# Performance work log

Hardware: AMD Instinct MI355X
Metric: run time of the kernel (lower is better)

The kernel has to match this reference:

```python
import jax, jax.numpy as jnp
import numpy as np

QN, QP = -8.0, 7.0  # int4 quantization range used by the cutlass q4 kernel
SCALE_DENOM = 11.269  # ~sqrt(127), from set_activation_scale


def _quant4(t, clip):
    # clip-based dynamic quantization to int4 grid (values kept in float)
    return jnp.clip(jnp.round(t / clip), QN, QP)


def setup_inputs() -> dict:
    key = jax.random.key(0)
    kx, ky = jax.random.split(key)
    x = jax.random.normal(kx, (4, 16, 1024, 256), dtype=jnp.float32)
    y = jax.random.normal(ky, (4, 16, 256, 1024), dtype=jnp.float32)
    # set_activation_scale: alpha = 2 * |t|.mean() / 11.269 (module uses x for both)
    x_clip = 2.0 * jnp.mean(jnp.abs(x)) / SCALE_DENOM
    y_clip = 2.0 * jnp.mean(jnp.abs(x)) / SCALE_DENOM
    return {"x": x, "y": y, "x_clip": x_clip, "y_clip": y_clip}


def reference(x, y, x_clip, y_clip):
    # quantize both operands to int4 grid, integer-grid matmul, dequant by clip scales
    qx = _quant4(x, x_clip)  # [B, H, M, K]
    qy = _quant4(y, y_clip)  # [B, H, K, N]
    out = jnp.einsum("bhmk,bhkn->bhmn", qx, qy)
    return out * x_clip * y_clip
```

## Files before the change

kernel.cpp:

```cpp
#include <hip/hip_runtime.h>

#define NBATCH 64
#define M_DIM  1024
#define K_DIM  256
#define N_DIM  1024

typedef __attribute__((ext_vector_type(4)))  int   i32x4;
typedef __attribute__((ext_vector_type(4)))  float f32x4;

union Pack16 { char c[16]; i32x4 i; };

__device__ __forceinline__ float quant4f(float v, float clip) {
    return fminf(fmaxf(rintf(v / clip), -8.0f), 7.0f);
}

__global__ __launch_bounds__(256) void quant_kernel(
        const float* __restrict__ x, const float* __restrict__ y,
        const float* __restrict__ xclip_p, const float* __restrict__ yclip_p,
        char* __restrict__ qx, char* __restrict__ qyT) {
    __shared__ float tile[64][65];
    const int bid = blockIdx.x;
    const int tid = threadIdx.x;

    if (bid < 4096) {
        const float clip = xclip_p[0];
        const int idx = (bid * 256 + tid) * 16;
        Pack16 o;
#pragma unroll
        for (int c = 0; c < 4; ++c) {
            f32x4 v = *(const f32x4*)(x + idx + c * 4);
#pragma unroll
            for (int j = 0; j < 4; ++j)
                o.c[c * 4 + j] = (char)(int)quant4f(v[j], clip);
        }
        *(i32x4*)(qx + idx) = o.i;
    } else {
        const float clip = yclip_p[0];
        const int b2 = bid - 4096;
        const int n0 = (b2 & 15) * 64;
        const int kb = (b2 >> 4) & 3;
        const int k0 = kb * 64;
        const int b  = b2 >> 6;
        const float* yb = y + (size_t)b * K_DIM * N_DIM;
        const int kl = tid >> 4;
        const int nq = (tid & 15) * 4;
#pragma unroll
        for (int i = 0; i < 4; ++i) {
            f32x4 v = *(const f32x4*)(yb + (size_t)(k0 + kl + i * 16) * N_DIM + n0 + nq);
#pragma unroll
            for (int j = 0; j < 4; ++j)
                tile[kl + i * 16][nq + j] = quant4f(v[j], clip);
        }
        __syncthreads();
        char* ob = qyT + ((size_t)b * 4 + kb) * 1024 * 64;
        const int nl = tid >> 2;
        const int kc = (tid & 3) * 16;
        Pack16 o;
#pragma unroll
        for (int j = 0; j < 16; ++j)
            o.c[j] = (char)(int)tile[kc + j][nl];
        *(i32x4*)(ob + (size_t)(n0 + nl) * 64 + kc) = o.i;
    }
}

#define GLD16(gp, lp) __builtin_amdgcn_global_load_lds(                         \
    (const __attribute__((address_space(1))) void*)(gp),                        \
    (__attribute__((address_space(3))) void*)(lp), 16, 0, 0)

__global__ __launch_bounds__(256, 4) void q4_gemm_kernel(
        const char* __restrict__ qx,
        const char* __restrict__ qyT,
        const float* __restrict__ xclip_p, const float* __restrict__ yclip_p,
        float* __restrict__ out) {
    const int p = blockIdx.x;
    const int l = (p & 7) * 512 + (p >> 3);
    const int b  = l >> 6;
    const int t  = l & 63;
    const int br = t >> 3;
    const int bc = t & 7;

    __shared__ __align__(16) char smem[32768];
    float (*Cst)[132] = (float (*)[132])smem;

    const int tid  = threadIdx.x;
    const int lane = tid & 63;
    const int wid  = tid >> 6;
    const int wr   = wid >> 1;
    const int wc   = wid & 1;

    const char* Abase = qx  + (size_t)b * M_DIM * K_DIM + (size_t)br * 128 * K_DIM;
    const char* Bbase = qyT + (size_t)b * 4 * 65536 + (size_t)bc * 128 * 64;

    const int row0  = tid >> 2;
    const int row1  = (tid + 256) >> 2;
    const int slot  = tid & 3;
    const int ks0   = (slot ^ (row0 & 3)) * 16;
    const int ks1   = (slot ^ (row1 & 3)) * 16;

    i32x4 acc[4][4] = {};

    const int lrow15 = lane & 15;
    const int s      = lane >> 4;

    {
        char* As = smem; char* Bs = smem + 8192;
        GLD16(Abase + (size_t)row0 * K_DIM + ks0, As + tid * 16);
        GLD16(Bbase + (size_t)row0 * 64 + ks0, Bs + tid * 16);
        GLD16(Abase + (size_t)row1 * K_DIM + ks1, As + (tid + 256) * 16);
        GLD16(Bbase + (size_t)row1 * 64 + ks1, Bs + (tid + 256) * 16);
    }
    __syncthreads();

#pragma unroll
    for (int kt = 0; kt < 4; ++kt) {
        char* As = smem + (kt & 1) * 16384;
        char* Bs = As + 8192;
        if (kt < 3) {
            const int ka = (kt + 1) * 64;
            const size_t kbb = (size_t)(kt + 1) * 65536;
            char* An = smem + ((kt + 1) & 1) * 16384;
            char* Bn = An + 8192;
            GLD16(Abase + (size_t)row0 * K_DIM + ka + ks0, An + tid * 16);
            GLD16(Bbase + kbb + (size_t)row0 * 64 + ks0, Bn + tid * 16);
            GLD16(Abase + (size_t)row1 * K_DIM + ka + ks1, An + (tid + 256) * 16);
            GLD16(Bbase + kbb + (size_t)row1 * 64 + ks1, Bn + (tid + 256) * 16);
        }

        i32x4 af[4], bf[4];
#pragma unroll
        for (int m = 0; m < 4; ++m) {
            int row = wr * 64 + m * 16 + lrow15;
            af[m] = *(const i32x4*)(As + row * 64 + ((s ^ (row & 3)) * 16));
        }
#pragma unroll
        for (int n = 0; n < 4; ++n) {
            int row = wc * 64 + n * 16 + lrow15;
            bf[n] = *(const i32x4*)(Bs + row * 64 + ((s ^ (row & 3)) * 16));
        }
#pragma unroll
        for (int m = 0; m < 4; ++m)
#pragma unroll
            for (int n = 0; n < 4; ++n)
                acc[m][n] = __builtin_amdgcn_mfma_i32_16x16x64_i8(
                                af[m], bf[n], acc[m][n], 0, 0, 0);
        __syncthreads();
    }

    const float scale = xclip_p[0] * yclip_p[0];
    const size_t cb = (size_t)b * M_DIM * N_DIM
                    + (size_t)(br * 128) * N_DIM + bc * 128;
    const int rsub = (lane >> 4) * 4;
    const int rdr  = tid >> 3;
    const int cdw0 = (tid & 7) * 4;

#pragma unroll
    for (int m = 0; m < 4; ++m) {
#pragma unroll
        for (int n = 0; n < 4; ++n)
#pragma unroll
            for (int j = 0; j < 4; ++j)
                Cst[wr * 16 + rsub + j][wc * 64 + n * 16 + lrow15] =
                    (float)acc[m][n][j] * scale;
        __syncthreads();
        const int grow = (rdr >> 4) * 64 + m * 16 + (rdr & 15);
#pragma unroll
        for (int i = 0; i < 4; ++i) {
            f32x4 v = *(const f32x4*)&Cst[rdr][cdw0 + i * 32];
            __builtin_nontemporal_store(
                v, (f32x4*)(out + cb + (size_t)grow * N_DIM + cdw0 + i * 32));
        }
        __syncthreads();
    }
}

extern "C" void kernel_launch(void* const* d_in, const int* in_sizes, int n_in,
                              void* d_out, int out_size, void* d_ws, size_t ws_size,
                              hipStream_t stream) {
    const float* x     = (const float*)d_in[0];
    const float* y     = (const float*)d_in[1];
    const float* xclip = (const float*)d_in[2];
    const float* yclip = (const float*)d_in[3];
    float* out = (float*)d_out;

    char* qx  = (char*)d_ws;
    char* qyT = qx + (size_t)NBATCH * M_DIM * K_DIM;

    quant_kernel<<<8192, 256, 0, stream>>>(x, y, xclip, yclip, qx, qyT);
    q4_gemm_kernel<<<4096, 256, 0, stream>>>(qx, qyT, xclip, yclip, out);
}
```

Before: 79.76 us.

## Fuse x quantization into GEMM tile loading, drop separate qx pass

The separate quantization of x is removed. The GEMM kernel now loads fp32 x tiles directly, quantizes them in registers, and stores packed int8 into swizzled LDS after the MFMA step, overlapping with compute. This avoids writing and rereading the int8 qx buffer. In exchange, each x tile is read in fp32 by every column block (4x the bytes per reuse), register pressure rises, and occupancy hint is lowered to 3.

Measured after the change: 99.69 us. +25.0%, slower.

```diff
diff --git a/kernel.cpp b/kernel.cpp
--- a/kernel.cpp
+++ b/kernel.cpp
@@ -14,61 +14,54 @@
     return fminf(fmaxf(rintf(v / clip), -8.0f), 7.0f);
 }
 
-__global__ __launch_bounds__(256) void quant_kernel(
-        const float* __restrict__ x, const float* __restrict__ y,
-        const float* __restrict__ xclip_p, const float* __restrict__ yclip_p,
-        char* __restrict__ qx, char* __restrict__ qyT) {
+__device__ __forceinline__ i32x4 quant_pack16(const f32x4* v, float clip) {
+    Pack16 o;
+#pragma unroll
+    for (int c = 0; c < 4; ++c)
+#pragma unroll
+        for (int j = 0; j < 4; ++j)
+            o.c[c * 4 + j] = (char)(int)quant4f(v[c][j], clip);
+    return o.i;
+}
+
+__global__ __launch_bounds__(256) void quant_y_kernel(
+        const float* __restrict__ y, const float* __restrict__ clip_p,
+        char* __restrict__ qyT) {
     __shared__ float tile[64][65];
     const int bid = blockIdx.x;
     const int tid = threadIdx.x;
-
-    if (bid < 4096) {
-        const float clip = xclip_p[0];
-        const int idx = (bid * 256 + tid) * 16;
-        Pack16 o;
-#pragma unroll
-        for (int c = 0; c < 4; ++c) {
-            f32x4 v = *(const f32x4*)(x + idx + c * 4);
-#pragma unroll
-            for (int j = 0; j < 4; ++j)
-                o.c[c * 4 + j] = (char)(int)quant4f(v[j], clip);
-        }
-        *(i32x4*)(qx + idx) = o.i;
-    } else {
-        const float clip = yclip_p[0];
-        const int b2 = bid - 4096;
-        const int n0 = (b2 & 15) * 64;
-        const int kb = (b2 >> 4) & 3;
-        const int k0 = kb * 64;
-        const int b  = b2 >> 6;
-        const float* yb = y + (size_t)b * K_DIM * N_DIM;
-        const int kl = tid >> 4;
-        const int nq = (tid & 15) * 4;
-#pragma unroll
-        for (int i = 0; i < 4; ++i) {
-            f32x4 v = *(const f32x4*)(yb + (size_t)(k0 + kl + i * 16) * N_DIM + n0 + nq);
-#pragma unroll
-            for (int j = 0; j < 4; ++j)
-                tile[kl + i * 16][nq + j] = quant4f(v[j], clip);
-        }
-        __syncthreads();
-        char* ob = qyT + ((size_t)b * 4 + kb) * 1024 * 64;
-        const int nl = tid >> 2;
-        const int kc = (tid & 3) * 16;
-        Pack16 o;
-#pragma unroll
-        for (int j = 0; j < 16; ++j)
-            o.c[j] = (char)(int)tile[kc + j][nl];
-        *(i32x4*)(ob + (size_t)(n0 + nl) * 64 + kc) = o.i;
-    }
+    const float clip = clip_p[0];
+    const int n0 = (bid & 15) * 64;
+    const int kb = (bid >> 4) & 3;
+    const int k0 = kb * 64;
+    const int b  = bid >> 6;
+    const float* yb = y + (size_t)b * K_DIM * N_DIM;
+    const int kl = tid >> 4;
+    const int nq = (tid & 15) * 4;
+#pragma unroll
+    for (int i = 0; i < 4; ++i) {
+        f32x4 v = *(const f32x4*)(yb + (size_t)(k0 + kl + i * 16) * N_DIM + n0 + nq);
+#pragma unroll
+        for (int j = 0; j < 4; ++j)
+            tile[kl + i * 16][nq + j] = quant4f(v[j], clip);
+    }
+    __syncthreads();
+    char* ob = qyT + ((size_t)b * 4 + kb) * 1024 * 64;
+    const int nl = tid >> 2;
+    const int kc = (tid & 3) * 16;
+    Pack16 o;
+#pragma unroll
+    for (int j = 0; j < 16; ++j)
+        o.c[j] = (char)(int)tile[kc + j][nl];
+    *(i32x4*)(ob + (size_t)(n0 + nl) * 64 + kc) = o.i;
 }
 
 #define GLD16(gp, lp) __builtin_amdgcn_global_load_lds(                         \
     (const __attribute__((address_space(1))) void*)(gp),                        \
     (__attribute__((address_space(3))) void*)(lp), 16, 0, 0)
 
-__global__ __launch_bounds__(256, 4) void q4_gemm_kernel(
-        const char* __restrict__ qx,
+__global__ __launch_bounds__(256, 3) void q4_gemm_kernel(
+        const float* __restrict__ x,
         const char* __restrict__ qyT,
         const float* __restrict__ xclip_p, const float* __restrict__ yclip_p,
         float* __restrict__ out) {
@@ -88,14 +81,18 @@
     const int wr   = wid >> 1;
     const int wc   = wid & 1;
 
-    const char* Abase = qx  + (size_t)b * M_DIM * K_DIM + (size_t)br * 128 * K_DIM;
-    const char* Bbase = qyT + (size_t)b * 4 * 65536 + (size_t)bc * 128 * 64;
-
-    const int row0  = tid >> 2;
-    const int row1  = (tid + 256) >> 2;
-    const int slot  = tid & 3;
-    const int ks0   = (slot ^ (row0 & 3)) * 16;
-    const int ks1   = (slot ^ (row1 & 3)) * 16;
+    const float* Axf  = x + (size_t)b * M_DIM * K_DIM + (size_t)br * 128 * K_DIM;
+    const char*  Bbase = qyT + (size_t)b * 4 * 65536 + (size_t)bc * 128 * 64;
+    const float  xclip = xclip_p[0];
+
+    const int row0 = tid >> 2;
+    const int row1 = row0 + 64;
+    const int slot = tid & 3;
+    const int ke   = slot * 16;
+    const int wd0  = (slot ^ (row0 & 3)) * 16;
+    const int wd1  = (slot ^ (row1 & 3)) * 16;
+    const int bs0  = wd0;
+    const int bs1  = wd1;
 
     i32x4 acc[4][4] = {};
 
@@ -104,10 +101,16 @@
 
     {
         char* As = smem; char* Bs = smem + 8192;
-        GLD16(Abase + (size_t)row0 * K_DIM + ks0, As + tid * 16);
-        GLD16(Bbase + (size_t)row0 * 64 + ks0, Bs + tid * 16);
-        GLD16(Abase + (size_t)row1 * K_DIM + ks1, As + (tid + 256) * 16);
-        GLD16(Bbase + (size_t)row1 * 64 + ks1, Bs + (tid + 256) * 16);
+        GLD16(Bbase + (size_t)row0 * 64 + bs0, Bs + tid * 16);
+        GLD16(Bbase + (size_t)row1 * 64 + bs1, Bs + (tid + 256) * 16);
+        f32x4 a0[4], a1[4];
+#pragma unroll
+        for (int j = 0; j < 4; ++j) {
+            a0[j] = *(const f32x4*)(Axf + (size_t)row0 * K_DIM + ke + j * 4);
+            a1[j] = *(const f32x4*)(Axf + (size_t)row1 * K_DIM + ke + j * 4);
+        }
+        *(i32x4*)(As + row0 * 64 + wd0) = quant_pack16(a0, xclip);
+        *(i32x4*)(As + row1 * 64 + wd1) = quant_pack16(a1, xclip);
     }
     __syncthreads();
 
@@ -115,15 +118,18 @@
     for (int kt = 0; kt < 4; ++kt) {
         char* As = smem + (kt & 1) * 16384;
         char* Bs = As + 8192;
+        f32x4 a0[4], a1[4];
         if (kt < 3) {
-            const int ka = (kt + 1) * 64;
+            const int    ka  = (kt + 1) * 64;
             const size_t kbb = (size_t)(kt + 1) * 65536;
-            char* An = smem + ((kt + 1) & 1) * 16384;
-            char* Bn = An + 8192;
-            GLD16(Abase + (size_t)row0 * K_DIM + ka + ks0, An + tid * 16);
-            GLD16(Bbase + kbb + (size_t)row0 * 64 + ks0, Bn + tid * 16);
-            GLD16(Abase + (size_t)row1 * K_DIM + ka + ks1, An + (tid + 256) * 16);
-            GLD16(Bbase + kbb + (size_t)row1 * 64 + ks1, Bn + (tid + 256) * 16);
+            char* Bn = smem + ((kt + 1) & 1) * 16384 + 8192;
+            GLD16(Bbase + kbb + (size_t)row0 * 64 + bs0, Bn + tid * 16);
+            GLD16(Bbase + kbb + (size_t)row1 * 64 + bs1, Bn + (tid + 256) * 16);
+#pragma unroll
+            for (int j = 0; j < 4; ++j) {
+                a0[j] = *(const f32x4*)(Axf + (size_t)row0 * K_DIM + ka + ke + j * 4);
+                a1[j] = *(const f32x4*)(Axf + (size_t)row1 * K_DIM + ka + ke + j * 4);
+            }
         }
 
         i32x4 af[4], bf[4];
@@ -143,10 +149,16 @@
             for (int n = 0; n < 4; ++n)
                 acc[m][n] = __builtin_amdgcn_mfma_i32_16x16x64_i8(
                                 af[m], bf[n], acc[m][n], 0, 0, 0);
+
+        if (kt < 3) {
+            char* An = smem + ((kt + 1) & 1) * 16384;
+            *(i32x4*)(An + row0 * 64 + wd0) = quant_pack16(a0, xclip);
+            *(i32x4*)(An + row1 * 64 + wd1) = quant_pack16(a1, xclip);
+        }
         __syncthreads();
     }
 
-    const float scale = xclip_p[0] * yclip_p[0];
+    const float scale = xclip * yclip_p[0];
     const size_t cb = (size_t)b * M_DIM * N_DIM
                     + (size_t)(br * 128) * N_DIM + bc * 128;
     const int rsub = (lane >> 4) * 4;
@@ -182,9 +194,8 @@
     const float* yclip = (const float*)d_in[3];
     float* out = (float*)d_out;
 
-    char* qx  = (char*)d_ws;
-    char* qyT = qx + (size_t)NBATCH * M_DIM * K_DIM;
-
-    quant_kernel<<<8192, 256, 0, stream>>>(x, y, xclip, yclip, qx, qyT);
-    q4_gemm_kernel<<<4096, 256, 0, stream>>>(qx, qyT, xclip, yclip, out);
-}
+    char* qyT = (char*)d_ws;
+
+    quant_y_kernel<<<4096, 256, 0, stream>>>(y, yclip, qyT);
+    q4_gemm_kernel<<<4096, 256, 0, stream>>>(x, qyT, xclip, yclip, out);
+}
```
